# Kernel optimization log

Hardware: AMD Instinct MI355X
Metric: run time of the kernel (lower is better)

The kernel has to match this reference:

```python
import jax, jax.numpy as jnp
import numpy as np

EPS = 1e-12  # torch F.normalize default eps


def setup_inputs() -> dict:
    key = jax.random.key(0)
    ks = jax.random.split(key, 7)
    dim, heads = 128, 8
    b, c, s, h, w = 2, dim, 3, 128, 128
    sc = 1.0 / np.sqrt(dim)
    return {
        "x": jax.random.normal(ks[0], (b, c, s, h, w), dtype=jnp.float32),
        "Wq": jax.random.normal(ks[1], (dim, dim), dtype=jnp.float32) * sc,
        "Wk": jax.random.normal(ks[2], (dim, dim), dtype=jnp.float32) * sc,
        "Wv": jax.random.normal(ks[3], (dim, dim), dtype=jnp.float32) * sc,
        "Wp": jax.random.normal(ks[4], (dim, dim), dtype=jnp.float32) * sc,
        "bp": jax.random.normal(ks[5], (dim,), dtype=jnp.float32) * 0.01,
        "rescale": jnp.ones((heads, 1, 1), dtype=jnp.float32),
    }


def _l2norm(t):
    # torch F.normalize(p=2, dim=-1): t / max(||t||, eps)
    n = jnp.sqrt(jnp.sum(t * t, axis=-1, keepdims=True))
    return t / jnp.maximum(n, EPS)


def reference(x, Wq, Wk, Wv, Wp, bp, rescale):
    b, c, s, h, w = x.shape
    heads = rescale.shape[0]
    d = c // heads
    n = h * w * s
    # [b,c,s,h,w] -> [b,h,w,s,c] -> [b, n, c]
    xt = jnp.transpose(x, (0, 3, 4, 2, 1)).reshape(b, n, c)
    # torch Linear: y = x @ W.T
    q = xt @ Wq.T
    k = xt @ Wk.T
    v = xt @ Wv.T
    # [b,n,heads,d] -> [b,heads,d,n] (channel attention: tokens along last axis)
    def to_heads(t):
        return jnp.transpose(t.reshape(b, n, heads, d), (0, 2, 3, 1))
    q, k, v = to_heads(q), to_heads(k), to_heads(v)
    q = _l2norm(q)
    k = _l2norm(k)
    # attn: [b,heads,d,d] = k @ q^T over token axis n
    attn = jnp.einsum('bhdn,bhen->bhde', k, q)
    attn = attn * rescale  # rescale broadcasts as [heads,1,1]
    attn = jax.nn.softmax(attn, axis=-1)
    out = jnp.einsum('bhde,bhen->bhdn', attn, v)  # [b,heads,d,n]
    # [b,heads,d,n] -> [b,n,heads*d]
    out = jnp.transpose(out, (0, 3, 1, 2)).reshape(b, n, c)
    out = out @ Wp.T + bp
    # [b,n,c] -> [b,h,w,s,c] -> [b,h,w,c,s] -> [b,c,s,h,w]
    out = out.reshape(b, h, w, s, c)
    out = jnp.transpose(out, (0, 1, 2, 4, 3))
    out = jnp.transpose(out, (0, 3, 4, 1, 2))
    return out
```

## Files before the change

kernel.cpp:

```cpp
#include <hip/hip_runtime.h>
#include <hip/hip_bf16.h>

typedef __bf16 bf16_t;
typedef __bf16 bf16x8 __attribute__((ext_vector_type(8)));
typedef float f32x4 __attribute__((ext_vector_type(4)));

#define NTOK 49152
#define CDIM 128
#define CHUNKS 192
#define KT 256
#define STEPS 8

__device__ inline f32x4 mfma16(bf16x8 a, bf16x8 b, f32x4 c) {
  return __builtin_amdgcn_mfma_f32_16x16x32_bf16(a, b, c, 0, 0, 0);
}

__global__ __launch_bounds__(256) void k1_gram(const float* __restrict__ x,
                                               float* __restrict__ part) {
  const int blk = blockIdx.x;
  const int b = blk / CHUNKS, chunk = blk % CHUNKS;
  const float* Xb = x + (size_t)b * CDIM * NTOK;
  const int tid = threadIdx.x, wave = tid >> 6, lane = tid & 63;
  const int r = lane & 15, quad = lane >> 4;

  __shared__ __align__(16) bf16_t tile[2][128 * 32];

  const int sch = tid >> 1, shalf = tid & 1;
  const float* gsrc = Xb + (size_t)sch * NTOK + chunk * KT + shalf * 16;

  f32x4 st[4];
#define STAGE_LOAD(step)                                   \
  {                                                        \
    const float* p_ = gsrc + (step) * 32;                  \
    st[0] = *(const f32x4*)(p_ + 0);                       \
    st[1] = *(const f32x4*)(p_ + 4);                       \
    st[2] = *(const f32x4*)(p_ + 8);                       \
    st[3] = *(const f32x4*)(p_ + 12);                      \
  }
#define STAGE_WRITE(buf)                                              \
  {                                                                   \
    bf16_t* t_ = &tile[buf][0];                                       \
    _Pragma("unroll")                                                 \
    for (int j_ = 0; j_ < 16; ++j_) {                                 \
      const int tok_ = shalf * 16 + j_;                               \
      const int c16_ = ((sch >> 4) << 6) + ((tok_ >> 3) << 4) + (sch & 15); \
      t_[c16_ * 8 + (tok_ & 7)] = (bf16_t)st[j_ >> 2][j_ & 3];        \
    }                                                                 \
  }

  f32x4 acc[2][8];
#pragma unroll
  for (int t = 0; t < 2; ++t)
#pragma unroll
    for (int j = 0; j < 8; ++j) acc[t][j] = (f32x4){0.f, 0.f, 0.f, 0.f};

  STAGE_LOAD(0);
  STAGE_WRITE(0);
  __syncthreads();

  for (int k = 0; k < STEPS; ++k) {
    const int buf = k & 1;
    if (k + 1 < STEPS) STAGE_LOAD(k + 1);
    bf16x8 frag[8];
#pragma unroll
    for (int g = 0; g < 8; ++g)
      frag[g] = *(const bf16x8*)&tile[buf][(g * 64 + lane) * 8];
    bf16x8 a0, a1;
    if (wave == 0)      { a0 = frag[0]; a1 = frag[1]; }
    else if (wave == 1) { a0 = frag[2]; a1 = frag[3]; }
    else if (wave == 2) { a0 = frag[4]; a1 = frag[5]; }
    else                { a0 = frag[6]; a1 = frag[7]; }
#pragma unroll
    for (int j = 0; j < 8; ++j) {
      acc[0][j] = mfma16(a0, frag[j], acc[0][j]);
      acc[1][j] = mfma16(a1, frag[j], acc[1][j]);
    }
    if (k + 1 < STEPS) STAGE_WRITE(1 - buf);
    __syncthreads();
  }
#undef STAGE_LOAD
#undef STAGE_WRITE

  float* pb = part + ((size_t)(b * CHUNKS + chunk) << 14);
#pragma unroll
  for (int t = 0; t < 2; ++t) {
#pragma unroll
    for (int j = 0; j < 8; ++j) {
#pragma unroll
      for (int reg = 0; reg < 4; ++reg) {
        const int row = wave * 32 + t * 16 + quad * 4 + reg;
        const int col = 16 * j + r;
        pb[row * 128 + col] = acc[t][j][reg];
      }
    }
  }
}

__global__ __launch_bounds__(256) void k2a_reduce(const float* __restrict__ part,
                                                  float* __restrict__ part2) {
  const int gid = blockIdx.x * 256 + threadIdx.x;
  const int e4 = gid & 4095, sl = (gid >> 12) & 7, b = gid >> 15;
  const float* p = part + ((size_t)(b * CHUNKS + sl * 24) << 14) + e4 * 4;
  f32x4 s = (f32x4){0.f, 0.f, 0.f, 0.f};
#pragma unroll 8
  for (int i = 0; i < 24; ++i) s += *(const f32x4*)(p + ((size_t)i << 14));
  *(f32x4*)(part2 + ((size_t)(b * 8 + sl) << 14) + e4 * 4) = s;
}

__global__ __launch_bounds__(256) void k2b_reduce(const float* __restrict__ part2,
                                                  float* __restrict__ S) {
  const int gid = blockIdx.x * 256 + threadIdx.x;
  const int e4 = gid & 4095, b = gid >> 12;
  f32x4 s = (f32x4){0.f, 0.f, 0.f, 0.f};
#pragma unroll
  for (int sl = 0; sl < 8; ++sl)
    s += *(const f32x4*)(part2 + ((size_t)(b * 8 + sl) << 14) + e4 * 4);
  *(f32x4*)(S + ((size_t)b << 14) + e4 * 4) = s;
}

__global__ __launch_bounds__(256) void k3_t(const float* __restrict__ S,
                                            const float* __restrict__ Wk,
                                            const float* __restrict__ Wq,
                                            float* __restrict__ Tm) {
  const int idx = blockIdx.x * 256 + threadIdx.x;
  const int j = idx & 127, i = (idx >> 7) & 127, t = (idx >> 14) & 1, b = idx >> 15;
  const f32x4* w4 = (const f32x4*)((t ? Wq : Wk) + i * 128);
  const f32x4* s4 = (const f32x4*)(S + (b << 14) + j * 128);
  float s = 0.f;
#pragma unroll 8
  for (int q = 0; q < 32; ++q) {
    const f32x4 a = w4[q], v = s4[q];
    s += a[0] * v[0] + a[1] * v[1] + a[2] * v[2] + a[3] * v[3];
  }
  Tm[idx] = s;
}

__global__ __launch_bounds__(256) void k3_attn(const float* __restrict__ Tm,
                                               const float* __restrict__ Wk,
                                               const float* __restrict__ Wq,
                                               const float* __restrict__ resc,
                                               float* __restrict__ attn) {
  const int blk = blockIdx.x;
  const int b = blk >> 3, h = blk & 7;
  const int tid = threadIdx.x, d = tid >> 4, e = tid & 15;
  const float* Tk = Tm + (size_t)(b * 2 + 0) * 16384;
  const float* Tq = Tm + (size_t)(b * 2 + 1) * 16384;

  const float* tkrow = Tk + (h * 16 + d) * 128;
  const float* wqrow = Wq + (h * 16 + e) * 128;
  float g = 0.f;
#pragma unroll 4
  for (int c = 0; c < 128; ++c) g += tkrow[c] * wqrow[c];

  __shared__ float sqk[16], sqq[16];
  if (e == 0) {
    const float* wkrow = Wk + (h * 16 + d) * 128;
    float s = 0.f;
    for (int c = 0; c < 128; ++c) s += tkrow[c] * wkrow[c];
    sqk[d] = s;
  }
  if (d == 0) {
    const float* tqrow = Tq + (h * 16 + e) * 128;
    float s = 0.f;
    for (int c = 0; c < 128; ++c) s += tqrow[c] * wqrow[c];
    sqq[e] = s;
  }
  __syncthreads();

  const float nk = fmaxf(sqrtf(fmaxf(sqk[d], 0.f)), 1e-12f);
  const float nq = fmaxf(sqrtf(fmaxf(sqq[e], 0.f)), 1e-12f);
  float pre = g / (nk * nq) * resc[h];

  float mx = pre;
#pragma unroll
  for (int m = 1; m < 16; m <<= 1) mx = fmaxf(mx, __shfl_xor(mx, m, 64));
  const float p = expf(pre - mx);
  float sum = p;
#pragma unroll
  for (int m = 1; m < 16; m <<= 1) sum += __shfl_xor(sum, m, 64);
  attn[blk * 256 + tid] = p / sum;
}

__global__ __launch_bounds__(256) void k3_p(const float* __restrict__ attn,
                                            const float* __restrict__ Wp,
                                            const float* __restrict__ Wv,
                                            bf16_t* __restrict__ Phi) {
  const int blk = blockIdx.x;
  const int b = blk >> 7, rrow = blk & 127;
  const int tid = threadIdx.x;
  __shared__ float M[128];
  if (tid < 128) {
    const int h = tid >> 4, e = tid & 15;
    const float* A = attn + (size_t)(b * 8 + h) * 256;
    const float* wp = Wp + rrow * 128 + h * 16;
    float m = 0.f;
#pragma unroll
    for (int d = 0; d < 16; ++d) m += wp[d] * A[d * 16 + e];
    M[tid] = m;
  }
  __syncthreads();
  if (tid < 128) {
    const int c = tid;
    float p = 0.f;
#pragma unroll 4
    for (int j = 0; j < 128; ++j) p += M[j] * Wv[j * 128 + c];
    Phi[((size_t)b << 14) + rrow * 128 + c] = (bf16_t)p;
  }
}

__global__ __launch_bounds__(256) void k4_out(const float* __restrict__ x,
                                              const bf16_t* __restrict__ Phi,
                                              const float* __restrict__ bp,
                                              float* __restrict__ out) {
  const int blk = blockIdx.x;
  const int b = blk / 768, tg = blk % 768;
  const float* Xb = x + (size_t)b * CDIM * NTOK;
  const bf16_t* Ph = Phi + ((size_t)b << 14);
  float* Ob = out + (size_t)b * CDIM * NTOK;
  const int tid = threadIdx.x, wave = tid >> 6, lane = tid & 63;
  const int r = lane & 15, quad = lane >> 4;
  const int tok0 = tg * 64;

  __shared__ __align__(16) bf16_t tile[128 * 64];

  {
    const int sch = tid >> 1, shalf = tid & 1;
    const float* p = Xb + (size_t)sch * NTOK + tok0 + shalf * 32;
    f32x4 st[8];
#pragma unroll
    for (int q = 0; q < 8; ++q) st[q] = *(const f32x4*)(p + q * 4);
    const int chunk_hi = ((sch >> 5) << 8) + (((sch >> 3) & 3) << 4);
    const int ei = sch & 7;
#pragma unroll
    for (int j = 0; j < 32; ++j) {
      const int tok = shalf * 32 + j;
      const int chunk = chunk_hi + ((tok >> 4) << 6) + (tok & 15);
      tile[chunk * 8 + ei] = (bf16_t)st[j >> 2][j & 3];
    }
  }
  __syncthreads();

  f32x4 acc[8];
#pragma unroll
  for (int m = 0; m < 8; ++m) acc[m] = (f32x4){0.f, 0.f, 0.f, 0.f};

#pragma unroll
  for (int step = 0; step < 4; ++step) {
    const bf16x8 bfr = *(const bf16x8*)&tile[(step * 256 + wave * 64 + lane) * 8];
#pragma unroll
    for (int m = 0; m < 8; ++m) {
      const bf16x8 ah = *(const bf16x8*)(Ph + (16 * m + r) * 128 + step * 32 + quad * 8);
      acc[m] = mfma16(ah, bfr, acc[m]);
    }
  }

  const int wtok = tok0 + wave * 16;
#pragma unroll
  for (int m = 0; m < 8; ++m) {
#pragma unroll
    for (int reg = 0; reg < 4; ++reg) {
      const int row = m * 16 + quad * 4 + reg;
      Ob[(size_t)row * NTOK + wtok + r] = acc[m][reg] + bp[row];
    }
  }
}

extern "C" void kernel_launch(void* const* d_in, const int* in_sizes, int n_in,
                              void* d_out, int out_size, void* d_ws, size_t ws_size,
                              hipStream_t stream) {
  const float* x    = (const float*)d_in[0];
  const float* Wq   = (const float*)d_in[1];
  const float* Wk   = (const float*)d_in[2];
  const float* Wv   = (const float*)d_in[3];
  const float* Wp   = (const float*)d_in[4];
  const float* bp   = (const float*)d_in[5];
  const float* resc = (const float*)d_in[6];
  float* out = (float*)d_out;

  char* ws = (char*)d_ws;
  float*  S    = (float*)(ws + 0);
  float*  Tm   = (float*)(ws + 131072);
  float*  attn = (float*)(ws + 393216);
  bf16_t* Phi  = (bf16_t*)(ws + 409600);
  float* part  = (float*)d_out;
  float* part2 = (float*)((char*)d_out + 25165824);

  k1_gram<<<2 * CHUNKS, 256, 0, stream>>>(x, part);
  k2a_reduce<<<256, 256, 0, stream>>>(part, part2);
  k2b_reduce<<<32, 256, 0, stream>>>(part2, S);
  k3_t<<<256, 256, 0, stream>>>(S, Wk, Wq, Tm);
  k3_attn<<<16, 256, 0, stream>>>(Tm, Wk, Wq, resc, attn);
  k3_p<<<256, 256, 0, stream>>>(attn, Wp, Wv, Phi);
  k4_out<<<1536, 256, 0, stream>>>(x, Phi, bp, out);
}
```

Baseline: 178.2 us.

## Vectorize gram staging and partial stores, retile chunks, coalesce output via LDS

The gram kernel now uses 128 larger chunks of 384 tokens instead of 192, writes LDS with bf16x4 vector stores, and runs a two-register-set ping-pong pipeline with lighter barriers. Partial Gram tiles are stored in MFMA fragment order as contiguous f32x4, and the second reduce remaps them back to row-major. The output kernel transposes its accumulators through padded LDS so global stores become coalesced f32x4 writes along tokens. Together these cut partial-sum traffic, LDS store count and scattered global writes, at the cost of fewer k1 blocks and extra LDS round trips in k4.

```diff
diff --git a/kernel.cpp b/kernel.cpp
--- a/kernel.cpp
+++ b/kernel.cpp
@@ -2,34 +2,40 @@
 #include <hip/hip_bf16.h>
 
 typedef __bf16 bf16_t;
+typedef __bf16 bf16x4 __attribute__((ext_vector_type(4)));
 typedef __bf16 bf16x8 __attribute__((ext_vector_type(8)));
 typedef float f32x4 __attribute__((ext_vector_type(4)));
 
 #define NTOK 49152
 #define CDIM 128
-#define CHUNKS 192
-#define KT 256
-#define STEPS 8
+#define CHUNKS 128
+#define KT 384
+#define STEPS 12
 
 __device__ inline f32x4 mfma16(bf16x8 a, bf16x8 b, f32x4 c) {
   return __builtin_amdgcn_mfma_f32_16x16x32_bf16(a, b, c, 0, 0, 0);
 }
+
+#define BARRIER() do { asm volatile("s_waitcnt lgkmcnt(0)" ::: "memory"); \
+    __builtin_amdgcn_s_barrier(); } while (0)
 
 __global__ __launch_bounds__(256) void k1_gram(const float* __restrict__ x,
                                                float* __restrict__ part) {
   const int blk = blockIdx.x;
-  const int b = blk / CHUNKS, chunk = blk % CHUNKS;
+  const int b = blk >> 7, chunk = blk & 127;
   const float* Xb = x + (size_t)b * CDIM * NTOK;
   const int tid = threadIdx.x, wave = tid >> 6, lane = tid & 63;
-  const int r = lane & 15, quad = lane >> 4;
 
   __shared__ __align__(16) bf16_t tile[2][128 * 32];
 
   const int sch = tid >> 1, shalf = tid & 1;
   const float* gsrc = Xb + (size_t)sch * NTOK + chunk * KT + shalf * 16;
-
-  f32x4 st[4];
-#define STAGE_LOAD(step)                                   \
+  const int c16base = ((sch >> 4) << 6) + (sch & 15);
+  const int cg0 = c16base + ((shalf * 2) << 4);
+  const int cg1 = c16base + ((shalf * 2 + 1) << 4);
+
+  f32x4 stA[4], stB[4];
+#define STAGE_LOAD(st, step)                               \
   {                                                        \
     const float* p_ = gsrc + (step) * 32;                  \
     st[0] = *(const f32x4*)(p_ + 0);                       \
@@ -37,15 +43,14 @@
     st[2] = *(const f32x4*)(p_ + 8);                       \
     st[3] = *(const f32x4*)(p_ + 12);                      \
   }
-#define STAGE_WRITE(buf)                                              \
-  {                                                                   \
-    bf16_t* t_ = &tile[buf][0];                                       \
-    _Pragma("unroll")                                                 \
-    for (int j_ = 0; j_ < 16; ++j_) {                                 \
-      const int tok_ = shalf * 16 + j_;                               \
-      const int c16_ = ((sch >> 4) << 6) + ((tok_ >> 3) << 4) + (sch & 15); \
-      t_[c16_ * 8 + (tok_ & 7)] = (bf16_t)st[j_ >> 2][j_ & 3];        \
-    }                                                                 \
+#define CVT4(v) (bf16x4){(bf16_t)(v)[0], (bf16_t)(v)[1], (bf16_t)(v)[2], (bf16_t)(v)[3]}
+#define STAGE_WRITE(st, buf)                               \
+  {                                                        \
+    bf16_t* t_ = &tile[buf][0];                            \
+    *(bf16x4*)&t_[cg0 * 8 + 0] = CVT4(st[0]);              \
+    *(bf16x4*)&t_[cg0 * 8 + 4] = CVT4(st[1]);              \
+    *(bf16x4*)&t_[cg1 * 8 + 0] = CVT4(st[2]);              \
+    *(bf16x4*)&t_[cg1 * 8 + 4] = CVT4(st[3]);              \
   }
 
   f32x4 acc[2][8];
@@ -54,68 +59,76 @@
 #pragma unroll
     for (int j = 0; j < 8; ++j) acc[t][j] = (f32x4){0.f, 0.f, 0.f, 0.f};
 
-  STAGE_LOAD(0);
-  STAGE_WRITE(0);
-  __syncthreads();
-
-  for (int k = 0; k < STEPS; ++k) {
-    const int buf = k & 1;
-    if (k + 1 < STEPS) STAGE_LOAD(k + 1);
-    bf16x8 frag[8];
-#pragma unroll
-    for (int g = 0; g < 8; ++g)
-      frag[g] = *(const bf16x8*)&tile[buf][(g * 64 + lane) * 8];
-    bf16x8 a0, a1;
-    if (wave == 0)      { a0 = frag[0]; a1 = frag[1]; }
-    else if (wave == 1) { a0 = frag[2]; a1 = frag[3]; }
-    else if (wave == 2) { a0 = frag[4]; a1 = frag[5]; }
-    else                { a0 = frag[6]; a1 = frag[7]; }
-#pragma unroll
-    for (int j = 0; j < 8; ++j) {
-      acc[0][j] = mfma16(a0, frag[j], acc[0][j]);
-      acc[1][j] = mfma16(a1, frag[j], acc[1][j]);
-    }
-    if (k + 1 < STEPS) STAGE_WRITE(1 - buf);
-    __syncthreads();
+#define MFMA_PHASE(buf)                                                     \
+  {                                                                         \
+    bf16x8 frag[8];                                                         \
+    _Pragma("unroll")                                                       \
+    for (int g = 0; g < 8; ++g)                                             \
+      frag[g] = *(const bf16x8*)&tile[buf][(g * 64 + lane) * 8];            \
+    bf16x8 a0, a1;                                                          \
+    if (wave == 0)      { a0 = frag[0]; a1 = frag[1]; }                     \
+    else if (wave == 1) { a0 = frag[2]; a1 = frag[3]; }                     \
+    else if (wave == 2) { a0 = frag[4]; a1 = frag[5]; }                     \
+    else                { a0 = frag[6]; a1 = frag[7]; }                     \
+    _Pragma("unroll")                                                       \
+    for (int j = 0; j < 8; ++j) {                                           \
+      acc[0][j] = mfma16(a0, frag[j], acc[0][j]);                           \
+      acc[1][j] = mfma16(a1, frag[j], acc[1][j]);                           \
+    }                                                                       \
+  }
+
+  STAGE_LOAD(stA, 0);
+  STAGE_WRITE(stA, 0);
+  STAGE_LOAD(stB, 1);
+  BARRIER();
+
+  for (int kk = 0; kk < STEPS; kk += 2) {
+    if (kk + 2 < STEPS) STAGE_LOAD(stA, kk + 2);
+    STAGE_WRITE(stB, 1);
+    MFMA_PHASE(0);
+    BARRIER();
+    if (kk + 3 < STEPS) STAGE_LOAD(stB, kk + 3);
+    if (kk + 2 < STEPS) STAGE_WRITE(stA, 0);
+    MFMA_PHASE(1);
+    BARRIER();
   }
 #undef STAGE_LOAD
 #undef STAGE_WRITE
+#undef MFMA_PHASE
 
   float* pb = part + ((size_t)(b * CHUNKS + chunk) << 14);
 #pragma unroll
-  for (int t = 0; t < 2; ++t) {
-#pragma unroll
-    for (int j = 0; j < 8; ++j) {
-#pragma unroll
-      for (int reg = 0; reg < 4; ++reg) {
-        const int row = wave * 32 + t * 16 + quad * 4 + reg;
-        const int col = 16 * j + r;
-        pb[row * 128 + col] = acc[t][j][reg];
-      }
-    }
-  }
+  for (int t = 0; t < 2; ++t)
+#pragma unroll
+    for (int j = 0; j < 8; ++j)
+      *(f32x4*)&pb[((((t * 8 + j) << 8) + tid) << 2)] = acc[t][j];
 }
 
 __global__ __launch_bounds__(256) void k2a_reduce(const float* __restrict__ part,
                                                   float* __restrict__ part2) {
   const int gid = blockIdx.x * 256 + threadIdx.x;
   const int e4 = gid & 4095, sl = (gid >> 12) & 7, b = gid >> 15;
-  const float* p = part + ((size_t)(b * CHUNKS + sl * 24) << 14) + e4 * 4;
+  const float* p = part + ((size_t)(b * CHUNKS + sl * 16) << 14) + e4 * 4;
   f32x4 s = (f32x4){0.f, 0.f, 0.f, 0.f};
 #pragma unroll 8
-  for (int i = 0; i < 24; ++i) s += *(const f32x4*)(p + ((size_t)i << 14));
+  for (int i = 0; i < 16; ++i) s += *(const f32x4*)(p + ((size_t)i << 14));
   *(f32x4*)(part2 + ((size_t)(b * 8 + sl) << 14) + e4 * 4) = s;
 }
 
 __global__ __launch_bounds__(256) void k2b_reduce(const float* __restrict__ part2,
                                                   float* __restrict__ S) {
   const int gid = blockIdx.x * 256 + threadIdx.x;
-  const int e4 = gid & 4095, b = gid >> 12;
+  const int g4 = gid & 4095, b = gid >> 12;
   f32x4 s = (f32x4){0.f, 0.f, 0.f, 0.f};
 #pragma unroll
   for (int sl = 0; sl < 8; ++sl)
-    s += *(const f32x4*)(part2 + ((size_t)(b * 8 + sl) << 14) + e4 * 4);
-  *(f32x4*)(S + ((size_t)b << 14) + e4 * 4) = s;
+    s += *(const f32x4*)(part2 + ((size_t)(b * 8 + sl) << 14) + g4 * 4);
+  const int tj = g4 >> 8, t = tj >> 3, j = tj & 7;
+  const int tid2 = g4 & 255, wave = tid2 >> 6, quad = (tid2 >> 4) & 3, r = tid2 & 15;
+  const int row0 = wave * 32 + t * 16 + quad * 4, col = j * 16 + r;
+  float* Sb = S + ((size_t)b << 14);
+#pragma unroll
+  for (int reg = 0; reg < 4; ++reg) Sb[(row0 + reg) * 128 + col] = s[reg];
 }
 
 __global__ __launch_bounds__(256) void k3_t(const float* __restrict__ S,
@@ -221,7 +234,9 @@
   const int r = lane & 15, quad = lane >> 4;
   const int tok0 = tg * 64;
 
-  __shared__ __align__(16) bf16_t tile[128 * 64];
+  __shared__ __align__(16) char smem[64 * 68 * 4];
+  bf16_t* tile = (bf16_t*)smem;
+  float* tbuf = (float*)smem;
 
   {
     const int sch = tid >> 1, shalf = tid & 1;
@@ -254,14 +269,26 @@
     }
   }
 
-  const int wtok = tok0 + wave * 16;
-#pragma unroll
-  for (int m = 0; m < 8; ++m) {
-#pragma unroll
-    for (int reg = 0; reg < 4; ++reg) {
-      const int row = m * 16 + quad * 4 + reg;
-      Ob[(size_t)row * NTOK + wtok + r] = acc[m][reg] + bp[row];
+  __syncthreads();
+#pragma unroll
+  for (int half = 0; half < 2; ++half) {
+#pragma unroll
+    for (int mm = 0; mm < 4; ++mm) {
+#pragma unroll
+      for (int reg = 0; reg < 4; ++reg)
+        tbuf[(mm * 16 + quad * 4 + reg) * 68 + wave * 16 + r] = acc[half * 4 + mm][reg];
     }
+    __syncthreads();
+#pragma unroll
+    for (int rep = 0; rep < 4; ++rep) {
+      const int idx = rep * 256 + tid, rloc = idx >> 4, g = idx & 15;
+      f32x4 v = *(const f32x4*)&tbuf[rloc * 68 + g * 4];
+      const int row = half * 64 + rloc;
+      const float bb = bp[row];
+      v[0] += bb; v[1] += bb; v[2] += bb; v[3] += bb;
+      *(f32x4*)&Ob[(size_t)row * NTOK + tok0 + g * 4] = v;
+    }
+    if (half == 0) __syncthreads();
   }
 }
 
@@ -283,7 +310,7 @@
   float*  attn = (float*)(ws + 393216);
   bf16_t* Phi  = (bf16_t*)(ws + 409600);
   float* part  = (float*)d_out;
-  float* part2 = (float*)((char*)d_out + 25165824);
+  float* part2 = (float*)((char*)d_out + 16777216);
 
   k1_gram<<<2 * CHUNKS, 256, 0, stream>>>(x, part);
   k2a_reduce<<<256, 256, 0, stream>>>(part, part2);
```

Measured after the change: 180.0 us. Within noise of the previous version (+1.0%).
